# Kernel optimization log

Hardware: AMD Instinct MI355X
Metric: run time of the kernel (lower is better)

The kernel has to match this reference:

```python
import jax, jax.numpy as jnp
import numpy as np

IGNORE_INDEX = 255
LOG_CLAMP = 100.0  # torch BCE clamps log at -100, so -log(x) <= 100


def _neg_log(x, cond):
    # BCE(x, 1) = -log(x), with the torch clamp log(x) >= -100.
    x_safe = jnp.where(cond, jnp.maximum(x, 1e-38), 1.0)
    return jnp.where(cond, jnp.minimum(-jnp.log(x_safe), LOG_CLAMP), 0.0)


def setup_inputs() -> dict:
    key = jax.random.key(0)
    k1, k2 = jax.random.split(key)
    B, C, H, W, D = 1, 20, 256, 256, 32
    pred = jax.random.normal(k1, (B, C, H, W, D), dtype=jnp.float32)
    target = jax.random.randint(k2, (B, H, W, D), 0, C, dtype=jnp.int64)
    return {"pred": pred, "target": target}


def reference(pred, target):
    C = pred.shape[1]
    p = jax.nn.softmax(pred, axis=1)                      # [B,C,H,W,D]
    mask = (target != IGNORE_INDEX)                        # [B,H,W,D]

    # Flatten voxels: [N, C] probs, [N] labels, [N] mask.
    p_flat = jnp.moveaxis(p, 1, -1).reshape(-1, C)
    t_flat = target.reshape(-1)
    m_flat = mask.reshape(-1).astype(p.dtype)
    t_safe = jnp.where(mask.reshape(-1), t_flat, 0).astype(jnp.int32)

    # Per-class reductions in one pass (replaces the per-class python loop):
    # nominator[c] = sum_{masked, t==c} p_c ; ct_count[c] = |{masked, t==c}|
    p_at_t = jnp.take_along_axis(p_flat, t_safe[:, None], axis=1)[:, 0] * m_flat
    nominator = jax.ops.segment_sum(p_at_t, t_safe, num_segments=C)
    ct_count = jax.ops.segment_sum(m_flat, t_safe, num_segments=C)
    sum_p = jnp.einsum('nc,n->c', p_flat, m_flat)          # sum of p_c over masked
    n_masked = jnp.sum(m_flat)

    neg_count = n_masked - ct_count                        # sum(1 - ct)
    spec_num = n_masked - sum_p - ct_count + nominator     # sum((1-p)(1-ct))

    valid = ct_count > 0
    prec = nominator / jnp.maximum(sum_p, 1e-38)
    rec = nominator / jnp.maximum(ct_count, 1.0)
    spec = spec_num / jnp.maximum(neg_count, 1.0)

    loss_c = (_neg_log(prec, valid & (sum_p > 0))
              + _neg_log(rec, valid)
              + _neg_log(spec, valid & (neg_count > 0)))
    count = jnp.sum(valid.astype(p.dtype))
    return jnp.sum(loss_c) / count
```

## Files before the change

### kernel.cpp

```cpp
#include <hip/hip_runtime.h>
#include <math.h>

#define NCLS 20
#define IGNORE_IDX 255
#define LOG2E 1.4426950408889634f
#define NBLK 512
#define NTHR 256

typedef float v4f __attribute__((ext_vector_type(4)));
typedef int v4i __attribute__((ext_vector_type(4)));

__device__ int g_cnt;

__device__ __forceinline__ float wave_reduce(float v) {
#pragma unroll
  for (int off = 32; off > 0; off >>= 1) v += __shfl_xor(v, off, 64);
  return v;
}

__device__ __forceinline__ float neg_log_clamped(float x, bool cond) {
  if (!cond) return 0.0f;
  float xs = fmaxf(x, 1e-38f);
  return fminf(-logf(xs), 100.0f);
}

__global__ __launch_bounds__(NTHR) void fused(const float* __restrict__ pred,
                                              const int* __restrict__ target,
                                              float* __restrict__ ws,
                                              float* __restrict__ out, int N) {
  __shared__ float s_acc[3 * NCLS];
  __shared__ float s_fin[64];
  __shared__ int s_last;
  const int tid = threadIdx.x;
  for (int i = tid; i < 3 * NCLS; i += NTHR) s_acc[i] = 0.0f;
  if (tid < 64) s_fin[tid] = 0.0f;
  __syncthreads();

  float acc[NCLS];
#pragma unroll
  for (int c = 0; c < NCLS; ++c) acc[c] = 0.0f;

  const int nq = N >> 2;
  const int tot = NBLK * NTHR;
  for (int q = blockIdx.x * NTHR + tid; q < nq; q += tot) {
    const int n = q << 2;
    v4f x[NCLS];
#pragma unroll
    for (int c = 0; c < NCLS; ++c)
      x[c] = __builtin_nontemporal_load(
          reinterpret_cast<const v4f*>(pred + (size_t)c * N + n));

    v4f m = x[0];
#pragma unroll
    for (int c = 1; c < NCLS; ++c) {
#pragma unroll
      for (int j = 0; j < 4; ++j) m[j] = fmaxf(m[j], x[c][j]);
    }

    const v4i t4 = *reinterpret_cast<const v4i*>(target + n);

    v4f s = (v4f)(0.0f);
    v4f pt = (v4f)(0.0f);
#pragma unroll
    for (int c = 0; c < NCLS; ++c) {
#pragma unroll
      for (int j = 0; j < 4; ++j) {
        x[c][j] = __builtin_amdgcn_exp2f((x[c][j] - m[j]) * LOG2E);
        s[j] += x[c][j];
        pt[j] = (c == t4[j]) ? x[c][j] : pt[j];
      }
    }

    float w[4];
    bool msk[4];
#pragma unroll
    for (int j = 0; j < 4; ++j) {
      msk[j] = (t4[j] != IGNORE_IDX);
      const float r = __builtin_amdgcn_rcpf(s[j]);
      w[j] = msk[j] ? r : 0.0f;
    }

#pragma unroll
    for (int c = 0; c < NCLS; ++c)
      acc[c] += x[c][0] * w[0] + x[c][1] * w[1] + x[c][2] * w[2] + x[c][3] * w[3];

#pragma unroll
    for (int j = 0; j < 4; ++j) {
      if (msk[j]) {
        atomicAdd(&s_acc[NCLS + t4[j]], pt[j] * w[j]);
        atomicAdd(&s_acc[2 * NCLS + t4[j]], 1.0f);
      }
    }
  }

#pragma unroll
  for (int c = 0; c < NCLS; ++c) {
    float v = wave_reduce(acc[c]);
    if ((tid & 63) == 0) atomicAdd(&s_acc[c], v);
  }
  __syncthreads();

  if (tid < 64)
    ws[(size_t)blockIdx.x * 64 + tid] = (tid < 3 * NCLS) ? s_acc[tid] : 0.0f;
  __threadfence();
  __syncthreads();

  if (tid == 0) {
    int old = __hip_atomic_fetch_add(&g_cnt, 1, __ATOMIC_ACQ_REL,
                                     __HIP_MEMORY_SCOPE_AGENT);
    s_last = (old == (int)gridDim.x - 1);
    if (s_last)
      __hip_atomic_store(&g_cnt, 0, __ATOMIC_RELAXED, __HIP_MEMORY_SCOPE_AGENT);
  }
  __syncthreads();
  if (!s_last) return;

  __threadfence();

  float a = 0.0f;
  const int total = NBLK * 64;
  for (int i = tid; i < total; i += NTHR) a += ws[i];
  atomicAdd(&s_fin[tid & 63], a);
  __syncthreads();

  if (tid < 64) {
    const float cnt = (tid < NCLS) ? s_fin[2 * NCLS + tid] : 0.0f;
    const float n_masked = wave_reduce(cnt);
    float loss = 0.0f, validf = 0.0f;
    if (tid < NCLS) {
      const float sump = s_fin[tid];
      const float nom = s_fin[NCLS + tid];
      const bool valid = cnt > 0.0f;
      const float prec = nom / fmaxf(sump, 1e-38f);
      const float rec = nom / fmaxf(cnt, 1.0f);
      const float negc = n_masked - cnt;
      const float specn = n_masked - sump - cnt + nom;
      const float spec = specn / fmaxf(negc, 1.0f);
      loss = neg_log_clamped(prec, valid && (sump > 0.0f)) +
             neg_log_clamped(rec, valid) +
             neg_log_clamped(spec, valid && (negc > 0.0f));
      validf = valid ? 1.0f : 0.0f;
    }
    loss = wave_reduce(loss);
    validf = wave_reduce(validf);
    if (tid == 0) out[0] = loss / validf;
  }
}

extern "C" void kernel_launch(void* const* d_in, const int* in_sizes, int n_in,
                              void* d_out, int out_size, void* d_ws, size_t ws_size,
                              hipStream_t stream) {
  const float* pred = (const float*)d_in[0];
  const int* target = (const int*)d_in[1];
  const int N = in_sizes[1];
  fused<<<NBLK, NTHR, 0, stream>>>(pred, target, (float*)d_ws, (float*)d_out, N);
}
```

Baseline: 296.9 us.

## Launch one block per quad tile and reduce partials into atomic slots

Replaces the fixed 512-block grid-stride loop with one block per 256 quads so each thread processes a single quad. Block partials are atomically added into 32 slots, zeroed by a memset before launch, so the last block sums only those 32 slots. A minimum-occupancy launch bound is added. This aims for more in-flight memory requests and a cheaper final reduction, at the cost of an extra memset launch and more global atomics.

```diff
diff --git a/kernel.cpp b/kernel.cpp
--- a/kernel.cpp
+++ b/kernel.cpp
@@ -4,8 +4,8 @@
 #define NCLS 20
 #define IGNORE_IDX 255
 #define LOG2E 1.4426950408889634f
-#define NBLK 512
 #define NTHR 256
+#define NSLOT 32
 
 typedef float v4f __attribute__((ext_vector_type(4)));
 typedef int v4i __attribute__((ext_vector_type(4)));
@@ -24,16 +24,15 @@
   return fminf(-logf(xs), 100.0f);
 }
 
-__global__ __launch_bounds__(NTHR) void fused(const float* __restrict__ pred,
-                                              const int* __restrict__ target,
-                                              float* __restrict__ ws,
-                                              float* __restrict__ out, int N) {
+__global__ __launch_bounds__(NTHR, 4) void fused(const float* __restrict__ pred,
+                                                 const int* __restrict__ target,
+                                                 float* __restrict__ ws,
+                                                 float* __restrict__ out, int N) {
   __shared__ float s_acc[3 * NCLS];
   __shared__ float s_fin[64];
   __shared__ int s_last;
   const int tid = threadIdx.x;
   for (int i = tid; i < 3 * NCLS; i += NTHR) s_acc[i] = 0.0f;
-  if (tid < 64) s_fin[tid] = 0.0f;
   __syncthreads();
 
   float acc[NCLS];
@@ -41,9 +40,11 @@
   for (int c = 0; c < NCLS; ++c) acc[c] = 0.0f;
 
   const int nq = N >> 2;
-  const int tot = NBLK * NTHR;
-  for (int q = blockIdx.x * NTHR + tid; q < nq; q += tot) {
+  const int q = blockIdx.x * NTHR + tid;
+
+  if (q < nq) {
     const int n = q << 2;
+    const v4i t4 = *reinterpret_cast<const v4i*>(target + n);
     v4f x[NCLS];
 #pragma unroll
     for (int c = 0; c < NCLS; ++c)
@@ -56,8 +57,6 @@
 #pragma unroll
       for (int j = 0; j < 4; ++j) m[j] = fmaxf(m[j], x[c][j]);
     }
-
-    const v4i t4 = *reinterpret_cast<const v4i*>(target + n);
 
     v4f s = (v4f)(0.0f);
     v4f pt = (v4f)(0.0f);
@@ -82,7 +81,7 @@
 
 #pragma unroll
     for (int c = 0; c < NCLS; ++c)
-      acc[c] += x[c][0] * w[0] + x[c][1] * w[1] + x[c][2] * w[2] + x[c][3] * w[3];
+      acc[c] = x[c][0] * w[0] + x[c][1] * w[1] + x[c][2] * w[2] + x[c][3] * w[3];
 
 #pragma unroll
     for (int j = 0; j < 4; ++j) {
@@ -100,8 +99,8 @@
   }
   __syncthreads();
 
-  if (tid < 64)
-    ws[(size_t)blockIdx.x * 64 + tid] = (tid < 3 * NCLS) ? s_acc[tid] : 0.0f;
+  if (tid < 3 * NCLS)
+    atomicAdd(&ws[(size_t)(blockIdx.x & (NSLOT - 1)) * 64 + tid], s_acc[tid]);
   __threadfence();
   __syncthreads();
 
@@ -115,12 +114,14 @@
   __syncthreads();
   if (!s_last) return;
 
-  __threadfence();
-
-  float a = 0.0f;
-  const int total = NBLK * 64;
-  for (int i = tid; i < total; i += NTHR) a += ws[i];
-  atomicAdd(&s_fin[tid & 63], a);
+  if (tid < 64) {
+    float a = 0.0f;
+#pragma unroll
+    for (int r = 0; r < NSLOT; ++r)
+      a += __hip_atomic_load(&ws[r * 64 + tid], __ATOMIC_RELAXED,
+                             __HIP_MEMORY_SCOPE_AGENT);
+    s_fin[tid] = a;
+  }
   __syncthreads();
 
   if (tid < 64) {
@@ -153,5 +154,9 @@
   const float* pred = (const float*)d_in[0];
   const int* target = (const int*)d_in[1];
   const int N = in_sizes[1];
-  fused<<<NBLK, NTHR, 0, stream>>>(pred, target, (float*)d_ws, (float*)d_out, N);
+  const int nq = N >> 2;
+  const int nblk = (nq + NTHR - 1) / NTHR;
+
+  hipMemsetAsync(d_ws, 0, NSLOT * 64 * sizeof(float), stream);
+  fused<<<nblk, NTHR, 0, stream>>>(pred, target, (float*)d_ws, (float*)d_out, N);
 }
```

New measurement: 441.0 us. 48.5% more time.
